# Kernel optimization log

Hardware: AMD Instinct MI355X
Metric: run time of the kernel (lower is better)

## Reference

```python
import jax, jax.numpy as jnp
import numpy as np

C_TANH = 10.0  # tanh_exploration


def _attn(q, e, Wq, bq, v, use_tanh):
    # q: [B,H]; e: [B,H,S] (pre-projected encoder refs); returns logits [B,S]
    qp = q @ Wq + bq
    u = jnp.einsum('h,bhs->bs', v, jnp.tanh(qp[:, :, None] + e))
    return C_TANH * jnp.tanh(u) if use_tanh else u


def setup_inputs() -> dict:
    key = jax.random.key(0)
    S, B, E, H = 256, 1024, 128, 128
    ks = jax.random.split(key, 16)
    r = lambda k, sh, s: jax.random.normal(k, sh, jnp.float32) * s
    bound = 1.0 / np.sqrt(H)
    return dict(
        decoder_input=r(ks[0], (B, E), 1.0),
        embedded_inputs=r(ks[1], (S, B, E), 1.0),
        hx=r(ks[2], (B, H), 1.0),
        cx=r(ks[3], (B, H), 1.0),
        context=r(ks[4], (S, B, H), 1.0),
        Wi=r(ks[5], (E, 4 * H), 0.05), bi=jnp.zeros((4 * H,), jnp.float32),
        Wh=r(ks[6], (H, 4 * H), 0.05), bh=jnp.zeros((4 * H,), jnp.float32),
        gWq=r(ks[7], (H, H), 0.05), gbq=jnp.zeros((H,), jnp.float32),
        gWr=r(ks[8], (H, H), 0.05), gbr=jnp.zeros((H,), jnp.float32),
        gv=jax.random.uniform(ks[9], (H,), jnp.float32, -bound, bound),
        pWq=r(ks[10], (H, H), 0.05), pbq=jnp.zeros((H,), jnp.float32),
        pWr=r(ks[11], (H, H), 0.05), pbr=jnp.zeros((H,), jnp.float32),
        pv=jax.random.uniform(ks[12], (H,), jnp.float32, -bound, bound),
    )


def reference(decoder_input, embedded_inputs, hx, cx, context,
              Wi, bi, Wh, bh, gWq, gbq, gWr, gbr, gv, pWq, pbq, pWr, pbr, pv):
    S, B, H = context.shape
    # project_ref (conv1d, k=1) is step-invariant: hoist out of the decode loop
    e_g = jnp.einsum('sbh,hg->bgs', context, gWr) + gbr[None, :, None]  # [B,H,S]
    e_p = jnp.einsum('sbh,hg->bgs', context, pWr) + pbr[None, :, None]
    NEG = jnp.float32(-jnp.inf)
    keys = jax.random.split(jax.random.key(42), S)
    arangeB = jnp.arange(B)

    def step(carry, key_t):
        x, hx_t, cx_t, mask, prev_idx, has_prev = carry
        # LSTM cell
        gates = x @ Wi + bi + hx_t @ Wh + bh
        i, f, g, o = jnp.split(gates, 4, axis=1)
        cy = jax.nn.sigmoid(f) * cx_t + jax.nn.sigmoid(i) * jnp.tanh(g)
        hy = jax.nn.sigmoid(o) * jnp.tanh(cy)
        # accumulate visited mask (no-op on the first step)
        maskk = mask | (jax.nn.one_hot(prev_idx, S, dtype=bool) & has_prev)
        # glimpse attention (use_tanh=False)
        gl = _attn(hy, e_g, gWq, gbq, gv, False)
        gl = jnp.where(maskk, NEG, gl)
        g_l = jnp.einsum('bgs,bs->bg', e_g, jax.nn.softmax(gl, axis=1))
        # pointer attention (use_tanh=True -> C*tanh)
        pl = _attn(g_l, e_p, pWq, pbq, pv, True)
        pl = jnp.where(maskk, NEG, pl)
        probs = jax.nn.softmax(pl, axis=1)
        idx = jax.random.categorical(key_t, pl)  # ~ probs.multinomial(1)
        x_next = embedded_inputs[idx, arangeB, :]
        return (x_next, hy, cy, maskk, idx, jnp.bool_(True)), (probs, idx)

    mask0 = jnp.zeros((B, S), dtype=bool)
    carry0 = (decoder_input, hx, cx, mask0, jnp.zeros((B,), jnp.int32), jnp.bool_(False))
    (_, hN, cN, _, _, _), (probs, idxs) = jax.lax.scan(step, carry0, keys)
    # ((outputs, selections), hidden)
    return probs, idxs, hN, cN
```

## Files before the change

### kernel.cpp

```cpp
#include <hip/hip_runtime.h>
#include <stdint.h>
#include <math.h>

#define S_ 256
#define B_ 1024
#define E_ 128
#define H_ 128
#define G4_ 512
#define NT 512

static const size_t OFF_P = 0;
static const size_t OFF_I = (size_t)S_ * B_ * S_;
static const size_t OFF_H = OFF_I + (size_t)S_ * B_;
static const size_t OFF_C = OFF_H + (size_t)B_ * H_;

template<typename T> struct alignas(2 * sizeof(T)) V2 { T x, y; };

__device__ __forceinline__ void tf2x32(uint32_t k0, uint32_t k1,
                                       uint32_t x0, uint32_t x1,
                                       uint32_t& o0, uint32_t& o1) {
  uint32_t ks2 = k0 ^ k1 ^ 0x1BD11BDAu;
#define RO_(v,r) (((v) << (r)) | ((v) >> (32-(r))))
#define RND_(r) { x0 += x1; x1 = RO_(x1,r); x1 ^= x0; }
  x0 += k0; x1 += k1;
  RND_(13) RND_(15) RND_(26) RND_(6)
  x0 += k1; x1 += ks2 + 1u;
  RND_(17) RND_(29) RND_(16) RND_(24)
  x0 += ks2; x1 += k0 + 2u;
  RND_(13) RND_(15) RND_(26) RND_(6)
  x0 += k0; x1 += k1 + 3u;
  RND_(17) RND_(29) RND_(16) RND_(24)
  x0 += k1; x1 += ks2 + 4u;
  RND_(13) RND_(15) RND_(26) RND_(6)
  x0 += ks2; x1 += k0 + 5u;
  o0 = x0; o1 = x1;
#undef RND_
#undef RO_
}

__device__ __forceinline__ double fexp(double x) {
  double t = x * 1.4426950408889634074;
  double n = rint(t);
  double r = __builtin_fma(n, -6.93147180369123816490e-01, x);
  r = __builtin_fma(n, -1.90821492927058770002e-10, r);
  double p = 2.08767569878681e-09;
  p = __builtin_fma(p, r, 2.50521083854417e-08);
  p = __builtin_fma(p, r, 2.75573192239859e-07);
  p = __builtin_fma(p, r, 2.75573192239859e-06);
  p = __builtin_fma(p, r, 2.48015873015873e-05);
  p = __builtin_fma(p, r, 1.98412698412698e-04);
  p = __builtin_fma(p, r, 1.38888888888889e-03);
  p = __builtin_fma(p, r, 8.33333333333333e-03);
  p = __builtin_fma(p, r, 4.16666666666667e-02);
  p = __builtin_fma(p, r, 1.66666666666667e-01);
  p = __builtin_fma(p, r, 5.0e-01);
  p = __builtin_fma(p, r, 1.0);
  p = __builtin_fma(p, r, 1.0);
  int ni = (int)n;
  double s = __longlong_as_double(((long long)(ni + 1023)) << 52);
  double res = p * s;
  return (x < -708.0) ? 0.0 : res;
}

__device__ __forceinline__ double ftanh(double x) {
  double a = fmin(fabs(x), 20.0);
  double w = fexp(-2.0 * a);
  double r = (1.0 - w) / (1.0 + w);
  return copysign(r, x);
}

__device__ __forceinline__ double fsigmoid(double x) {
  return 1.0 / (1.0 + fexp(-x));
}

__global__ void diag_write(float* out, float code) {
  if (threadIdx.x == 0 && blockIdx.x == 0) out[OFF_I] = code;
}

template<typename ETg, typename ETp, typename ETe>
__global__ __launch_bounds__(256) void precompute_e(
    const float* __restrict__ ctx,
    const float* __restrict__ gWr, const float* __restrict__ gbr,
    const float* __restrict__ pWr, const float* __restrict__ pbr,
    ETg* __restrict__ Eg, ETp* __restrict__ Ep, ETe* __restrict__ Elt) {
  __shared__ float cb[64][129];
  const int b = blockIdx.x;
  const int tid = threadIdx.x;
  const int sl = tid & 63;
  const int gq = tid >> 6;

  for (int s0 = 0; s0 < S_; s0 += 64) {
    __syncthreads();
    for (int i = tid; i < 64 * H_; i += 256) {
      int r = i >> 7, h = i & 127;
      cb[r][h] = ctx[((size_t)(s0 + r) * B_ + b) * H_ + h];
    }
    __syncthreads();
    const int s = s0 + sl;
    for (int g0 = 0; g0 < H_; g0 += 4) {
      int g = g0 + gq;
      double a = 0.0, a2 = 0.0;
#pragma unroll 8
      for (int h = 0; h < H_; ++h) {
        double c = (double)cb[sl][h];
        a  = fma(c, (double)gWr[h * H_ + g], a);
        a2 = fma(c, (double)pWr[h * H_ + g], a2);
      }
      double e1 = a + (double)gbr[g];
      double e2 = a2 + (double)pbr[g];
      size_t idx = ((size_t)b * H_ + g) * S_ + s;
      Eg[idx] = (ETg)fexp(-2.0 * e1);
      Ep[idx] = (ETp)fexp(-2.0 * e2);
      Elt[((size_t)b * S_ + s) * H_ + g] = (ETe)e1;
    }
  }
}

template<typename ETg, typename ETp, typename ETe>
__global__ __launch_bounds__(NT) void decoder_main(
    const float* __restrict__ dec, const float* __restrict__ emb,
    const float* __restrict__ hx0, const float* __restrict__ cx0,
    const float* __restrict__ Wi, const float* __restrict__ bi,
    const float* __restrict__ Wh, const float* __restrict__ bh,
    const float* __restrict__ gWq, const float* __restrict__ gbq,
    const float* __restrict__ gv,
    const float* __restrict__ pWq, const float* __restrict__ pbq,
    const float* __restrict__ pv,
    const ETg* __restrict__ Eg_g, const ETp* __restrict__ Ep_g,
    const ETe* __restrict__ Elt_g,
    float* __restrict__ out) {
  __shared__ double gates[G4_];
  __shared__ double red0[NT];
  __shared__ double red1[NT];
  __shared__ double eq[H_], eq2[H_], glv[H_];
  __shared__ double sh[H_], sc[H_];
  __shared__ float  sx[E_];
  __shared__ double gl[S_];
  __shared__ double wbuf[S_];
  __shared__ double plv[S_];
  __shared__ double pex[S_];
  __shared__ float  gvs[H_], pvs[H_];
  __shared__ float  msk[S_];
  __shared__ uint32_t kk0[S_], kk1[S_];
  __shared__ double redM[4];
  __shared__ double redA[4];
  __shared__ int    redI[4];
  __shared__ int s_idx;

  const int b = blockIdx.x;
  const int tid = threadIdx.x;

  if (tid < H_) {
    sh[tid] = (double)hx0[b * H_ + tid];
    sc[tid] = (double)cx0[b * H_ + tid];
    gvs[tid] = gv[tid]; pvs[tid] = pv[tid];
  } else if (tid < 2 * H_) {
    sx[tid - 128] = dec[b * E_ + (tid - 128)];
  }
  if (tid < S_) {
    msk[tid] = 0.f;
    uint32_t a0, a1;
    tf2x32(0u, 42u, 0u, (uint32_t)tid, a0, a1);
    kk0[tid] = a0; kk1[tid] = a1;
  }
  const double bi_c = (double)bi[tid];
  const double bh_c = (double)bh[tid];
  const double gbq_c = (tid < H_) ? (double)gbq[tid] : 0.0;
  const double pbq_c = (tid < H_) ? (double)pbq[tid] : 0.0;
  const ETg* Eg_b  = Eg_g  + (size_t)b * H_ * S_;
  const ETp* Ep_b  = Ep_g  + (size_t)b * H_ * S_;
  const ETe* Elt_b = Elt_g + (size_t)b * S_ * H_;
  const int sc2 = tid & 127;
  const int hq  = tid >> 7;
  __syncthreads();

  for (int t = 0; t < S_; ++t) {
    {
      double a = 0.0;
      const float* WiT = Wi + tid;
#pragma unroll 8
      for (int k = 0; k < E_; ++k) a = fma((double)sx[k], (double)WiT[(size_t)k * G4_], a);
      a += bi_c;
      const float* WhT = Wh + tid;
#pragma unroll 8
      for (int k = 0; k < H_; ++k) a = fma(sh[k], (double)WhT[(size_t)k * G4_], a);
      gates[tid] = a + bh_c;
    }
    __syncthreads();
    if (tid < H_) {
      double si = fsigmoid(gates[tid]);
      double sf = fsigmoid(gates[H_ + tid]);
      double tg = ftanh(gates[2 * H_ + tid]);
      double so = fsigmoid(gates[3 * H_ + tid]);
      double cn = sf * sc[tid] + si * tg;
      double hn = so * ftanh(cn);
      sc[tid] = cn; sh[tid] = hn;
      if (t == S_ - 1) {
        out[OFF_H + (size_t)b * H_ + tid] = (float)hn;
        out[OFF_C + (size_t)b * H_ + tid] = (float)cn;
      }
    }
    __syncthreads();
    if (tid < H_) {
      double a = 0.0;
      const float* wq = gWq + tid;
#pragma unroll 8
      for (int k = 0; k < H_; ++k) a = fma(sh[k], (double)wq[k * H_], a);
      eq[tid] = fexp(-2.0 * (a + gbq_c));
    }
    __syncthreads();
    {
      const V2<ETg>* egp = reinterpret_cast<const V2<ETg>*>(Eg_b)
                           + (size_t)hq * 32 * (S_ / 2);
      double a0 = 0.0, a1 = 0.0;
#pragma unroll 8
      for (int hh = 0; hh < 32; ++hh) {
        int h = hq * 32 + hh;
        V2<ETg> w2 = egp[hh * (S_ / 2) + sc2];
        double eqh = eq[h];
        double gvh = (double)gvs[h];
        double W0 = eqh * (double)w2.x;
        double W1 = eqh * (double)w2.y;
        double rd = 1.0 / ((1.0 + W0) * (1.0 + W1));
        a0 = fma(gvh, (1.0 - W0) * (1.0 + W1) * rd, a0);
        a1 = fma(gvh, (1.0 - W1) * (1.0 + W0) * rd, a1);
      }
      red0[tid] = a0; red1[tid] = a1;
    }
    __syncthreads();
    if (tid < 128) {
      int s0 = 2 * tid, s1 = s0 + 1;
      double v0 = (red0[tid] + red0[tid + 128]) + (red0[tid + 256] + red0[tid + 384]);
      double v1 = (red1[tid] + red1[tid + 128]) + (red1[tid + 256] + red1[tid + 384]);
      gl[s0] = (msk[s0] != 0.f) ? -INFINITY : v0;
      gl[s1] = (msk[s1] != 0.f) ? -INFINITY : v1;
    }
    __syncthreads();
    if (tid < S_) {
      double v = gl[tid];
      for (int o = 32; o; o >>= 1) v = fmax(v, __shfl_xor(v, o));
      if ((tid & 63) == 0) redM[tid >> 6] = v;
    }
    __syncthreads();
    {
      double m = fmax(fmax(redM[0], redM[1]), fmax(redM[2], redM[3]));
      if (tid < S_) pex[tid] = fexp(gl[tid] - m);
    }
    __syncthreads();
    if (tid < S_) {
      double sv = pex[tid];
      for (int o = 32; o; o >>= 1) sv += __shfl_xor(sv, o);
      if ((tid & 63) == 0) redM[tid >> 6] = sv;
    }
    __syncthreads();
    {
      double ssum = (redM[0] + redM[1]) + (redM[2] + redM[3]);
      if (tid < S_) wbuf[tid] = pex[tid] / ssum;
    }
    __syncthreads();
    if (tid < H_) {
      double a = 0.0;
#pragma unroll 8
      for (int s = 0; s < S_; ++s)
        a = fma((double)Elt_b[(size_t)s * H_ + tid], wbuf[s], a);
      glv[tid] = a;
    }
    __syncthreads();
    if (tid < H_) {
      double a = 0.0;
      const float* wq = pWq + tid;
#pragma unroll 8
      for (int k = 0; k < H_; ++k) a = fma(glv[k], (double)wq[k * H_], a);
      eq2[tid] = fexp(-2.0 * (a + pbq_c));
    }
    __syncthreads();
    {
      const V2<ETp>* epp = reinterpret_cast<const V2<ETp>*>(Ep_b)
                           + (size_t)hq * 32 * (S_ / 2);
      double a0 = 0.0, a1 = 0.0;
#pragma unroll 8
      for (int hh = 0; hh < 32; ++hh) {
        int h = hq * 32 + hh;
        V2<ETp> w2 = epp[hh * (S_ / 2) + sc2];
        double eqh = eq2[h];
        double pvh = (double)pvs[h];
        double W0 = eqh * (double)w2.x;
        double W1 = eqh * (double)w2.y;
        double rd = 1.0 / ((1.0 + W0) * (1.0 + W1));
        a0 = fma(pvh, (1.0 - W0) * (1.0 + W1) * rd, a0);
        a1 = fma(pvh, (1.0 - W1) * (1.0 + W0) * rd, a1);
      }
      red0[tid] = a0; red1[tid] = a1;
    }
    __syncthreads();
    if (tid < 128) {
      int s0 = 2 * tid, s1 = s0 + 1;
      double u0 = (red0[tid] + red0[tid + 128]) + (red0[tid + 256] + red0[tid + 384]);
      double u1 = (red1[tid] + red1[tid + 128]) + (red1[tid + 256] + red1[tid + 384]);
      plv[s0] = (msk[s0] != 0.f) ? -INFINITY : (10.0 * ftanh(u0));
      plv[s1] = (msk[s1] != 0.f) ? -INFINITY : (10.0 * ftanh(u1));
    }
    __syncthreads();
    if (tid < S_) {
      double v = plv[tid];
      for (int o = 32; o; o >>= 1) v = fmax(v, __shfl_xor(v, o));
      if ((tid & 63) == 0) redM[tid >> 6] = v;
    }
    __syncthreads();
    {
      double m2 = fmax(fmax(redM[0], redM[1]), fmax(redM[2], redM[3]));
      if (tid < S_) pex[tid] = fexp(plv[tid] - m2);
    }
    __syncthreads();
    if (tid < S_) {
      double sv = pex[tid];
      for (int o = 32; o; o >>= 1) sv += __shfl_xor(sv, o);
      if ((tid & 63) == 0) redM[tid >> 6] = sv;
    }
    __syncthreads();
    {
      double ssum2 = (redM[0] + redM[1]) + (redM[2] + redM[3]);
      if (tid < S_) out[OFF_P + ((size_t)t * B_ + b) * S_ + tid] = (float)(pex[tid] / ssum2);
    }
    if (tid < S_) {
      double zval; int zidx;
      uint32_t j = (uint32_t)(b * S_ + tid);
      uint32_t r0, r1;
      tf2x32(kk0[t], kk1[t], 0u, j, r0, r1);
      uint32_t bits = r0 ^ r1;
      float f = __uint_as_float((bits >> 9) | 0x3f800000u) - 1.0f;
      float u = fmaxf(f, 1.17549435082228751e-38f);
      double gmb = -log(-log((double)u));
      zval = gmb + plv[tid]; zidx = tid;
      for (int o = 32; o; o >>= 1) {
        double ov = __shfl_xor(zval, o);
        int    oi = __shfl_xor(zidx, o);
        if (ov > zval || (ov == zval && oi < zidx)) { zval = ov; zidx = oi; }
      }
      if ((tid & 63) == 0) { redA[tid >> 6] = zval; redI[tid >> 6] = zidx; }
    }
    __syncthreads();
    if (tid == 0) {
      double bv = redA[0]; int bx = redI[0];
#pragma unroll
      for (int w = 1; w < 4; ++w) {
        if (redA[w] > bv || (redA[w] == bv && redI[w] < bx)) { bv = redA[w]; bx = redI[w]; }
      }
      s_idx = bx;
      msk[bx] = 1.0f;
      out[OFF_I + (size_t)t * B_ + b] = (float)bx;
    }
    __syncthreads();
    if (tid < E_) sx[tid] = emb[((size_t)s_idx * B_ + b) * E_ + tid];
    __syncthreads();
  }
}

extern "C" void kernel_launch(void* const* d_in, const int* in_sizes, int n_in,
                              void* d_out, int out_size, void* d_ws, size_t ws_size,
                              hipStream_t stream) {
  const float* dec = (const float*)d_in[0];
  const float* emb = (const float*)d_in[1];
  const float* hx  = (const float*)d_in[2];
  const float* cx  = (const float*)d_in[3];
  const float* ctx = (const float*)d_in[4];
  const float* Wi  = (const float*)d_in[5];
  const float* bi  = (const float*)d_in[6];
  const float* Wh  = (const float*)d_in[7];
  const float* bh  = (const float*)d_in[8];
  const float* gWq = (const float*)d_in[9];
  const float* gbq = (const float*)d_in[10];
  const float* gWr = (const float*)d_in[11];
  const float* gbr = (const float*)d_in[12];
  const float* gv  = (const float*)d_in[13];
  const float* pWq = (const float*)d_in[14];
  const float* pbq = (const float*)d_in[15];
  const float* pWr = (const float*)d_in[16];
  const float* pbr = (const float*)d_in[17];
  const float* pv  = (const float*)d_in[18];
  float* out = (float*)d_out;
  char* w = (char*)d_ws;

  const size_t n_e = (size_t)B_ * H_ * S_;

  if (ws_size >= n_e * 12) {
    float* Eg = (float*)w;
    float* Ep = (float*)(w + n_e * 4);
    float* El = (float*)(w + n_e * 8);
    precompute_e<float,float,float><<<dim3(B_), dim3(256), 0, stream>>>(
        ctx, gWr, gbr, pWr, pbr, Eg, Ep, El);
    decoder_main<float,float,float><<<dim3(B_), dim3(NT), 0, stream>>>(
        dec, emb, hx, cx, Wi, bi, Wh, bh, gWq, gbq, gv, pWq, pbq, pv, Eg, Ep, El, out);
  } else {
    diag_write<<<dim3(1), dim3(64), 0, stream>>>(out, 700000.0f + (float)(ws_size >> 20));
  }
}
```

Before: 31.51 ms.

## Batch four tanh reciprocals per divide and parallelize glimpse context sum

The attention inner loops now handle four sequence positions per thread and share one double-precision reciprocal across all four tanh evaluations, where before one reciprocal covered two. This halves the divides per element at the cost of more registers and a wider eight-way shared reduction. The glimpse-weighted context sum also moves from 128 threads looping over all 256 positions to all 512 threads each covering a 64-position slice, followed by a shared-memory reduction. That adds one barrier in exchange for more parallelism.

```diff
diff --git a/kernel.cpp b/kernel.cpp
--- a/kernel.cpp
+++ b/kernel.cpp
@@ -15,6 +15,7 @@
 static const size_t OFF_C = OFF_H + (size_t)B_ * H_;
 
 template<typename T> struct alignas(2 * sizeof(T)) V2 { T x, y; };
+template<typename T> struct alignas(4 * sizeof(T)) V4 { T x, y, z, w; };
 
 __device__ __forceinline__ void tf2x32(uint32_t k0, uint32_t k1,
                                        uint32_t x0, uint32_t x1,
@@ -130,8 +131,7 @@
     const ETe* __restrict__ Elt_g,
     float* __restrict__ out) {
   __shared__ double gates[G4_];
-  __shared__ double red0[NT];
-  __shared__ double red1[NT];
+  __shared__ double red[4][NT];
   __shared__ double eq[H_], eq2[H_], glv[H_];
   __shared__ double sh[H_], sc[H_];
   __shared__ float  sx[E_];
@@ -170,8 +170,8 @@
   const ETg* Eg_b  = Eg_g  + (size_t)b * H_ * S_;
   const ETp* Ep_b  = Ep_g  + (size_t)b * H_ * S_;
   const ETe* Elt_b = Elt_g + (size_t)b * S_ * H_;
-  const int sc2 = tid & 127;
-  const int hq  = tid >> 7;
+  const int sq = tid & 63;
+  const int ho = tid >> 6;
   __syncthreads();
 
   for (int t = 0; t < S_; ++t) {
@@ -210,30 +210,38 @@
     }
     __syncthreads();
     {
-      const V2<ETg>* egp = reinterpret_cast<const V2<ETg>*>(Eg_b)
-                           + (size_t)hq * 32 * (S_ / 2);
-      double a0 = 0.0, a1 = 0.0;
-#pragma unroll 8
-      for (int hh = 0; hh < 32; ++hh) {
-        int h = hq * 32 + hh;
-        V2<ETg> w2 = egp[hh * (S_ / 2) + sc2];
+      const V4<ETg>* egp = reinterpret_cast<const V4<ETg>*>(Eg_b)
+                           + (size_t)ho * 16 * (S_ / 4);
+      double a0 = 0.0, a1 = 0.0, a2 = 0.0, a3 = 0.0;
+#pragma unroll 8
+      for (int hh = 0; hh < 16; ++hh) {
+        int h = ho * 16 + hh;
+        V4<ETg> w4 = egp[hh * (S_ / 4) + sq];
         double eqh = eq[h];
         double gvh = (double)gvs[h];
-        double W0 = eqh * (double)w2.x;
-        double W1 = eqh * (double)w2.y;
-        double rd = 1.0 / ((1.0 + W0) * (1.0 + W1));
-        a0 = fma(gvh, (1.0 - W0) * (1.0 + W1) * rd, a0);
-        a1 = fma(gvh, (1.0 - W1) * (1.0 + W0) * rd, a1);
-      }
-      red0[tid] = a0; red1[tid] = a1;
-    }
-    __syncthreads();
-    if (tid < 128) {
-      int s0 = 2 * tid, s1 = s0 + 1;
-      double v0 = (red0[tid] + red0[tid + 128]) + (red0[tid + 256] + red0[tid + 384]);
-      double v1 = (red1[tid] + red1[tid + 128]) + (red1[tid + 256] + red1[tid + 384]);
-      gl[s0] = (msk[s0] != 0.f) ? -INFINITY : v0;
-      gl[s1] = (msk[s1] != 0.f) ? -INFINITY : v1;
+        double W0 = eqh * (double)w4.x;
+        double W1 = eqh * (double)w4.y;
+        double W2 = eqh * (double)w4.z;
+        double W3 = eqh * (double)w4.w;
+        double p0 = 1.0 + W0, p1 = 1.0 + W1, p2 = 1.0 + W2, p3 = 1.0 + W3;
+        double P01 = p0 * p1, P23 = p2 * p3;
+        double rd = 1.0 / (P01 * P23);
+        double q01 = P23 * rd;
+        double q23 = P01 * rd;
+        a0 = fma(gvh, (1.0 - W0) * p1 * q01, a0);
+        a1 = fma(gvh, (1.0 - W1) * p0 * q01, a1);
+        a2 = fma(gvh, (1.0 - W2) * p3 * q23, a2);
+        a3 = fma(gvh, (1.0 - W3) * p2 * q23, a3);
+      }
+      red[0][tid] = a0; red[1][tid] = a1; red[2][tid] = a2; red[3][tid] = a3;
+    }
+    __syncthreads();
+    if (tid < S_) {
+      int j = tid & 3, q = tid >> 2;
+      const double* rj = red[j];
+      double v = ((rj[q] + rj[64 + q]) + (rj[128 + q] + rj[192 + q]))
+               + ((rj[256 + q] + rj[320 + q]) + (rj[384 + q] + rj[448 + q]));
+      gl[tid] = (msk[tid] != 0.f) ? -INFINITY : v;
     }
     __syncthreads();
     if (tid < S_) {
@@ -258,13 +266,18 @@
       if (tid < S_) wbuf[tid] = pex[tid] / ssum;
     }
     __syncthreads();
-    if (tid < H_) {
+    {
+      int g = tid & 127, sq4 = tid >> 7;
+      const ETe* col = Elt_b + (size_t)(sq4 * 64) * H_ + g;
+      const double* wp = wbuf + sq4 * 64;
       double a = 0.0;
 #pragma unroll 8
-      for (int s = 0; s < S_; ++s)
-        a = fma((double)Elt_b[(size_t)s * H_ + tid], wbuf[s], a);
-      glv[tid] = a;
-    }
+      for (int s = 0; s < 64; ++s)
+        a = fma((double)col[(size_t)s * H_], wp[s], a);
+      red[0][tid] = a;
+    }
+    __syncthreads();
+    if (tid < H_) glv[tid] = (red[0][tid] + red[0][tid + 128]) + (red[0][tid + 256] + red[0][tid + 384]);
     __syncthreads();
     if (tid < H_) {
       double a = 0.0;
@@ -275,30 +288,38 @@
     }
     __syncthreads();
     {
-      const V2<ETp>* epp = reinterpret_cast<const V2<ETp>*>(Ep_b)
-                           + (size_t)hq * 32 * (S_ / 2);
-      double a0 = 0.0, a1 = 0.0;
-#pragma unroll 8
-      for (int hh = 0; hh < 32; ++hh) {
-        int h = hq * 32 + hh;
-        V2<ETp> w2 = epp[hh * (S_ / 2) + sc2];
+      const V4<ETp>* epp = reinterpret_cast<const V4<ETp>*>(Ep_b)
+                           + (size_t)ho * 16 * (S_ / 4);
+      double a0 = 0.0, a1 = 0.0, a2 = 0.0, a3 = 0.0;
+#pragma unroll 8
+      for (int hh = 0; hh < 16; ++hh) {
+        int h = ho * 16 + hh;
+        V4<ETp> w4 = epp[hh * (S_ / 4) + sq];
         double eqh = eq2[h];
         double pvh = (double)pvs[h];
-        double W0 = eqh * (double)w2.x;
-        double W1 = eqh * (double)w2.y;
-        double rd = 1.0 / ((1.0 + W0) * (1.0 + W1));
-        a0 = fma(pvh, (1.0 - W0) * (1.0 + W1) * rd, a0);
-        a1 = fma(pvh, (1.0 - W1) * (1.0 + W0) * rd, a1);
-      }
-      red0[tid] = a0; red1[tid] = a1;
-    }
-    __syncthreads();
-    if (tid < 128) {
-      int s0 = 2 * tid, s1 = s0 + 1;
-      double u0 = (red0[tid] + red0[tid + 128]) + (red0[tid + 256] + red0[tid + 384]);
-      double u1 = (red1[tid] + red1[tid + 128]) + (red1[tid + 256] + red1[tid + 384]);
-      plv[s0] = (msk[s0] != 0.f) ? -INFINITY : (10.0 * ftanh(u0));
-      plv[s1] = (msk[s1] != 0.f) ? -INFINITY : (10.0 * ftanh(u1));
+        double W0 = eqh * (double)w4.x;
+        double W1 = eqh * (double)w4.y;
+        double W2 = eqh * (double)w4.z;
+        double W3 = eqh * (double)w4.w;
+        double p0 = 1.0 + W0, p1 = 1.0 + W1, p2 = 1.0 + W2, p3 = 1.0 + W3;
+        double P01 = p0 * p1, P23 = p2 * p3;
+        double rd = 1.0 / (P01 * P23);
+        double q01 = P23 * rd;
+        double q23 = P01 * rd;
+        a0 = fma(pvh, (1.0 - W0) * p1 * q01, a0);
+        a1 = fma(pvh, (1.0 - W1) * p0 * q01, a1);
+        a2 = fma(pvh, (1.0 - W2) * p3 * q23, a2);
+        a3 = fma(pvh, (1.0 - W3) * p2 * q23, a3);
+      }
+      red[0][tid] = a0; red[1][tid] = a1; red[2][tid] = a2; red[3][tid] = a3;
+    }
+    __syncthreads();
+    if (tid < S_) {
+      int j = tid & 3, q = tid >> 2;
+      const double* rj = red[j];
+      double u = ((rj[q] + rj[64 + q]) + (rj[128 + q] + rj[192 + q]))
+               + ((rj[256 + q] + rj[320 + q]) + (rj[384 + q] + rj[448 + q]));
+      plv[tid] = (msk[tid] != 0.f) ? -INFINITY : (10.0 * ftanh(u));
     }
     __syncthreads();
     if (tid < S_) {
```

New measurement: 43.09 ms. 36.8% more time.
